# Kernel tuning notes

Hardware: AMD Instinct MI355X
Metric: run time of the kernel (lower is better)

Reference implementation:

```python
import jax, jax.numpy as jnp
import numpy as np

N = 4096
IN_FEATS = 64
HIDDEN = 128
STEPS = 3
SCALE = 3.0
LJ_EPS = 0.1
LJ_SIGMA = 3.5
LJ_MIX = 0.1  # 'auto' branch: pot = exp(-r/scale)*relu(score) + 0.1*lj
LN_EPS = 1e-5


def setup_inputs() -> dict:
    key = jax.random.key(0)
    ks = jax.random.split(key, 12)
    x = jax.random.normal(ks[0], (N, IN_FEATS), dtype=jnp.float32)
    # sparse-ish 0/1 adjacency (float, as multiplied in the torch code)
    adj = (jax.random.uniform(ks[1], (N, N)) < 0.02).astype(jnp.float32)
    # positive pairwise distances in Angstrom-like range
    dist_mat = jax.random.uniform(ks[2], (N, N), dtype=jnp.float32) * 10.0 + 0.5
    s_in = 1.0 / np.sqrt(IN_FEATS)
    s_h = 1.0 / np.sqrt(HIDDEN)
    s_2h = 1.0 / np.sqrt(2 * HIDDEN)
    params = {
        'W_in': jax.random.uniform(ks[3], (IN_FEATS, HIDDEN), minval=-s_in, maxval=s_in),
        'b_in': jnp.zeros((HIDDEN,), jnp.float32),
        'W_msg': jax.random.uniform(ks[4], (HIDDEN, HIDDEN), minval=-s_h, maxval=s_h),
        'b_msg': jnp.zeros((HIDDEN,), jnp.float32),
        'W_u1': jax.random.uniform(ks[5], (2 * HIDDEN, HIDDEN), minval=-s_2h, maxval=s_2h),
        'b_u1': jnp.zeros((HIDDEN,), jnp.float32),
        'W_u2': jax.random.uniform(ks[6], (HIDDEN, HIDDEN), minval=-s_h, maxval=s_h),
        'b_u2': jnp.zeros((HIDDEN,), jnp.float32),
        'gamma': jnp.ones((HIDDEN,), jnp.float32),
        'beta': jnp.zeros((HIDDEN,), jnp.float32),
    }
    return {'x': x, 'adj': adj, 'dist_mat': dist_mat, **params}


def _layernorm(x, gamma, beta):
    mu = jnp.mean(x, axis=-1, keepdims=True)
    var = jnp.mean(jnp.square(x - mu), axis=-1, keepdims=True)
    return (x - mu) * jax.lax.rsqrt(var + LN_EPS) * gamma + beta


def reference(x, adj, dist_mat, W_in, b_in, W_msg, b_msg, W_u1, b_u1, W_u2, b_u2, gamma, beta):
    h = x @ W_in + b_in  # (n, hidden)
    # distance-only terms are loop-invariant
    r_safe = jnp.clip(dist_mat, 1e-6, None)
    sr6 = (LJ_SIGMA / r_safe) ** 6
    lj = 4.0 * LJ_EPS * (sr6 * sr6 - sr6)          # (n, n)
    decay = jnp.exp(-dist_mat / SCALE)             # (n, n)
    pot_const = LJ_MIX * lj                        # 'auto' branch constant part
    for _ in range(STEPS):
        # torch code computes msg_lin(h) but never uses it (dead code) -> skipped
        # pot_scalar[i,j] = <h_i, h_j>, computed without (n,n,d) materialization
        pot_scalar = h @ h.T                       # (n, n)
        pot = decay * jax.nn.relu(pot_scalar) + pot_const
        # m_i = sum_j pot[i,j]*adj[i,j]*h_j == masked-weighted matmul
        m = (pot * adj) @ h                        # (n, hidden)
        concat = jnp.concatenate([h, m], axis=-1)  # (n, 2*hidden)
        delta = jax.nn.relu(concat @ W_u1 + b_u1) @ W_u2 + b_u2
        h = _layernorm(h + delta, gamma, beta)
    return h
```

## Files before the change

### kernel.cpp

```cpp
#include <hip/hip_runtime.h>
#include <hip/hip_bf16.h>

#define NN   4096
#define HID  128
#define INFE 64
#define KE   160
#define KMAX 192
#define CH   64
#define RPB  4

typedef unsigned short u16;
typedef unsigned int   u32;

__device__ __forceinline__ float bfu(u16 u) { return __uint_as_float(((u32)u) << 16); }
__device__ __forceinline__ float bflo(u32 w){ return __uint_as_float(w << 16); }
__device__ __forceinline__ float bfhi(u32 w){ return __uint_as_float(w & 0xffff0000u); }
__device__ __forceinline__ u16 f2b(float f) { __hip_bfloat16 h = __float2bfloat16(f); return *(u16*)&h; }

__global__ __launch_bounds__(128) void k_h0(
    const float* __restrict__ x, const float* __restrict__ Win, const float* __restrict__ bin,
    float* __restrict__ hdst, u16* __restrict__ bdst)
{
    __shared__ float xl[INFE];
    const int r = blockIdx.x;
    const int d = threadIdx.x;
    if (d < INFE) xl[d] = x[(size_t)r*INFE + d];
    __syncthreads();
    float acc = bin[d];
    #pragma unroll 8
    for (int k = 0; k < INFE; ++k)
        acc = fmaf(xl[k], Win[k*HID + d], acc);
    hdst[(size_t)r*HID + d] = acc;
    bdst[(size_t)r*HID + d] = f2b(acc);
}

__global__ __launch_bounds__(256) void k_build(
    const float* __restrict__ adj, const float* __restrict__ dist,
    float4* __restrict__ edges, int* __restrict__ nnzp)
{
    __shared__ int cnt[2];
    __shared__ int   cl[2][KE];
    __shared__ float ca[2][KE];
    const int r0 = blockIdx.x * 2;
    const int t  = threadIdx.x;
    if (t < 2) cnt[t] = 0;
    __syncthreads();
    float4 av[2][4];
    #pragma unroll
    for (int rr = 0; rr < 2; ++rr) {
        const float4* arow = (const float4*)(adj + (size_t)(r0+rr)*NN);
        #pragma unroll
        for (int q = 0; q < 4; ++q) av[rr][q] = arow[t + 256*q];
    }
    #pragma unroll
    for (int rr = 0; rr < 2; ++rr) {
        #pragma unroll
        for (int q = 0; q < 4; ++q) {
            float a4[4] = {av[rr][q].x, av[rr][q].y, av[rr][q].z, av[rr][q].w};
            if (a4[0] != 0.f || a4[1] != 0.f || a4[2] != 0.f || a4[3] != 0.f) {
                #pragma unroll
                for (int u = 0; u < 4; ++u) {
                    if (a4[u] != 0.f) {
                        int pos = atomicAdd(&cnt[rr], 1);
                        if (pos < KE) { cl[rr][pos] = 4*(t + 256*q) + u; ca[rr][pos] = a4[u]; }
                    }
                }
            }
        }
    }
    __syncthreads();
    #pragma unroll
    for (int rr = 0; rr < 2; ++rr) {
        const int n  = cnt[rr] < KE ? cnt[rr] : KE;
        const int np = (n + 15) / 16 * 16;
        float4* erow = edges + (size_t)(r0+rr)*KE;
        for (int i = n + t; i < np; i += 256)
            erow[i] = make_float4(__int_as_float(0), 0.f, 0.f, 0.f);
        const float* drow = dist + (size_t)(r0+rr)*NN;
        for (int i = t; i < n; i += 256) {
            int   c = cl[rr][i];
            float a = ca[rr][i];
            float d  = fmaxf(drow[c], 1e-6f);
            float dw1 = a * __expf(-d * (1.0f/3.0f));
            float tt = 3.5f / d, t2 = tt*tt, t6 = t2*t2*t2;
            float dw2 = a * 0.04f * (t6*t6 - t6);
            erow[i] = make_float4(__int_as_float(c), dw1, dw2, 0.f);
        }
        if (t == 0) nnzp[r0+rr] = np;
    }
}

__global__ __launch_bounds__(256) void k_fstep(
    const float4* __restrict__ edges, const int* __restrict__ nnzp,
    const float* __restrict__ h, const u16* __restrict__ hb,
    const float* __restrict__ Wu1, const float* __restrict__ bu1,
    const float* __restrict__ Wu2, const float* __restrict__ bu2,
    const float* __restrict__ gam, const float* __restrict__ bet,
    float* __restrict__ hout, u16* __restrict__ bout)
{
    __shared__ __align__(16) float4 eds[RPB][KE];
    __shared__ int npl[RPB];
    __shared__ __align__(16) float hs[RPB][HID];
    __shared__ __align__(16) float ms[RPB][HID];
    __shared__ __align__(16) float h1s[RPB][HID];
    __shared__ float hn[RPB][HID];
    const int t    = threadIdx.x;
    const int w    = t >> 6;
    const int lane = t & 63;
    const int g    = lane >> 5;
    const int j    = lane & 31;
    const int r0   = blockIdx.x * RPB;
    const int r    = r0 + w;

    if (t < RPB) npl[t] = nnzp[r0 + t];
    const float4 hi4 = *(const float4*)(h + (size_t)r*HID + 4*j);
    if (g == 0) *(float4*)&hs[w][4*j] = hi4;
    __syncthreads();
    #pragma unroll
    for (int rr = 0; rr < RPB; ++rr) {
        const float4* er = edges + (size_t)(r0+rr)*KE;
        for (int i = t; i < npl[rr]; i += 256) eds[rr][i] = er[i];
    }
    __syncthreads();

    const int np = npl[w];
    float4 macc = make_float4(0.f, 0.f, 0.f, 0.f);
    for (int e0 = 0; e0 < np; e0 += 16) {
        float4 ed[8]; uint2 hj16[8]; float p[8];
        #pragma unroll
        for (int q = 0; q < 8; ++q) ed[q] = eds[w][e0 + g + 2*q];
        #pragma unroll
        for (int q = 0; q < 8; ++q) {
            int c = __float_as_int(ed[q].x);
            hj16[q] = *(const uint2*)(hb + (size_t)c*HID + 4*j);
        }
        float4 hjf[8];
        #pragma unroll
        for (int q = 0; q < 8; ++q) {
            hjf[q].x = bflo(hj16[q].x); hjf[q].y = bfhi(hj16[q].x);
            hjf[q].z = bflo(hj16[q].y); hjf[q].w = bfhi(hj16[q].y);
            p[q] = hi4.x*hjf[q].x;
            p[q] = fmaf(hi4.y, hjf[q].y, p[q]);
            p[q] = fmaf(hi4.z, hjf[q].z, p[q]);
            p[q] = fmaf(hi4.w, hjf[q].w, p[q]);
        }
        #pragma unroll
        for (int mask = 1; mask <= 16; mask <<= 1) {
            #pragma unroll
            for (int q = 0; q < 8; ++q) p[q] += __shfl_xor(p[q], mask);
        }
        #pragma unroll
        for (int q = 0; q < 8; ++q) {
            float wq = fmaf(ed[q].y, fmaxf(p[q], 0.f), ed[q].z);
            macc.x = fmaf(wq, hjf[q].x, macc.x);
            macc.y = fmaf(wq, hjf[q].y, macc.y);
            macc.z = fmaf(wq, hjf[q].z, macc.z);
            macc.w = fmaf(wq, hjf[q].w, macc.w);
        }
    }
    macc.x += __shfl_xor(macc.x, 32);
    macc.y += __shfl_xor(macc.y, 32);
    macc.z += __shfl_xor(macc.z, 32);
    macc.w += __shfl_xor(macc.w, 32);
    if (g == 0) *(float4*)&ms[w][4*j] = macc;
    __syncthreads();

    {
        const int half = t >> 7;
        const int d    = t & 127;
        const int ra = 2*half, rb = ra + 1;
        float bb = bu1[d];
        float a0 = bb, a1 = bb;
        for (int k = 0; k < HID; k += 4) {
            float w0 = Wu1[(k+0)*HID + d], w1 = Wu1[(k+1)*HID + d];
            float w2 = Wu1[(k+2)*HID + d], w3 = Wu1[(k+3)*HID + d];
            float4 caa = *(const float4*)&hs[ra][k];
            float4 cbb = *(const float4*)&hs[rb][k];
            a0 = fmaf(caa.x,w0,a0); a0 = fmaf(caa.y,w1,a0); a0 = fmaf(caa.z,w2,a0); a0 = fmaf(caa.w,w3,a0);
            a1 = fmaf(cbb.x,w0,a1); a1 = fmaf(cbb.y,w1,a1); a1 = fmaf(cbb.z,w2,a1); a1 = fmaf(cbb.w,w3,a1);
        }
        for (int k = 0; k < HID; k += 4) {
            float w0 = Wu1[(HID+k+0)*HID + d], w1 = Wu1[(HID+k+1)*HID + d];
            float w2 = Wu1[(HID+k+2)*HID + d], w3 = Wu1[(HID+k+3)*HID + d];
            float4 caa = *(const float4*)&ms[ra][k];
            float4 cbb = *(const float4*)&ms[rb][k];
            a0 = fmaf(caa.x,w0,a0); a0 = fmaf(caa.y,w1,a0); a0 = fmaf(caa.z,w2,a0); a0 = fmaf(caa.w,w3,a0);
            a1 = fmaf(cbb.x,w0,a1); a1 = fmaf(cbb.y,w1,a1); a1 = fmaf(cbb.z,w2,a1); a1 = fmaf(cbb.w,w3,a1);
        }
        h1s[ra][d] = fmaxf(a0, 0.f);
        h1s[rb][d] = fmaxf(a1, 0.f);
    }
    __syncthreads();
    {
        const int half = t >> 7;
        const int d    = t & 127;
        const int ra = 2*half, rb = ra + 1;
        float bb = bu2[d];
        float b0 = bb, b1 = bb;
        for (int k = 0; k < HID; k += 4) {
            float w0 = Wu2[(k+0)*HID + d], w1 = Wu2[(k+1)*HID + d];
            float w2 = Wu2[(k+2)*HID + d], w3 = Wu2[(k+3)*HID + d];
            float4 caa = *(const float4*)&h1s[ra][k];
            float4 cbb = *(const float4*)&h1s[rb][k];
            b0 = fmaf(caa.x,w0,b0); b0 = fmaf(caa.y,w1,b0); b0 = fmaf(caa.z,w2,b0); b0 = fmaf(caa.w,w3,b0);
            b1 = fmaf(cbb.x,w0,b1); b1 = fmaf(cbb.y,w1,b1); b1 = fmaf(cbb.z,w2,b1); b1 = fmaf(cbb.w,w3,b1);
        }
        hn[ra][d] = hs[ra][d] + b0;
        hn[rb][d] = hs[rb][d] + b1;
    }
    __syncthreads();
    {
        float v0 = hn[w][lane], v1 = hn[w][lane + 64];
        float s = v0 + v1;
        #pragma unroll
        for (int mask = 1; mask <= 32; mask <<= 1) s += __shfl_xor(s, mask);
        float mu = s * (1.0f/128.0f);
        float z0 = v0 - mu, z1 = v1 - mu;
        float vv = fmaf(z0, z0, z1*z1);
        #pragma unroll
        for (int mask = 1; mask <= 32; mask <<= 1) vv += __shfl_xor(vv, mask);
        float rstd = rsqrtf(vv * (1.0f/128.0f) + 1e-5f);
        float o0 = fmaf(z0 * rstd, gam[lane],      bet[lane]);
        float o1 = fmaf(z1 * rstd, gam[lane + 64], bet[lane + 64]);
        hout[(size_t)r*HID + lane]      = o0;
        hout[(size_t)r*HID + lane + 64] = o1;
        bout[(size_t)r*HID + lane]      = f2b(o0);
        bout[(size_t)r*HID + lane + 64] = f2b(o1);
    }
}

template<bool SB, bool DB>
__global__ __launch_bounds__(128) void k_step(
    const float* __restrict__ adj, const float* __restrict__ dist,
    const void* hsrc, void* hdst,
    const float* __restrict__ Wu1, const float* __restrict__ bu1,
    const float* __restrict__ Wu2, const float* __restrict__ bu2,
    const float* __restrict__ gam, const float* __restrict__ bet)
{
    __shared__ int   cnt4[RPB];
    __shared__ int   cl[RPB][KMAX];
    __shared__ float w1l[RPB][KMAX], w2l[RPB][KMAX];
    __shared__ __align__(16) float hs4[RPB][HID];
    __shared__ __align__(16) float hj[CH][HID + 1];
    __shared__ float pl[CH];
    __shared__ __align__(16) float ms[RPB][HID];
    __shared__ __align__(16) float h1s[RPB][HID];
    __shared__ float hn[RPB][HID];
    const int r0 = blockIdx.x * RPB;
    const int t  = threadIdx.x;
    const u16*   s16 = (const u16*)hsrc;
    const float* s32 = (const float*)hsrc;
    if (t < RPB) cnt4[t] = 0;
    for (int i = t; i < RPB*HID; i += 128) {
        int rr = i >> 7, d = i & 127;
        hs4[rr][d] = SB ? bfu(s16[(size_t)(r0+rr)*HID + d]) : s32[(size_t)(r0+rr)*HID + d];
    }
    __syncthreads();
    for (int idx = t; idx < RPB*(NN/4); idx += 128) {
        int rr = idx >> 10, c4 = idx & 1023;
        float4 a4 = ((const float4*)(adj + (size_t)(r0+rr)*NN))[c4];
        if (a4.x != 0.f || a4.y != 0.f || a4.z != 0.f || a4.w != 0.f) {
            const float* drow = dist + (size_t)(r0+rr)*NN;
            float av4[4] = {a4.x, a4.y, a4.z, a4.w};
            #pragma unroll
            for (int q = 0; q < 4; ++q) {
                float av = av4[q];
                if (av != 0.f) {
                    int c = 4*c4 + q;
                    float d  = fmaxf(drow[c], 1e-6f);
                    float dw1 = av * __expf(-d * (1.0f/3.0f));
                    float tt = 3.5f / d, t2 = tt*tt, t6 = t2*t2*t2;
                    float dw2 = av * 0.04f * (t6*t6 - t6);
                    int pos = atomicAdd(&cnt4[rr], 1);
                    if (pos < KMAX) { cl[rr][pos] = c; w1l[rr][pos] = dw1; w2l[rr][pos] = dw2; }
                }
            }
        }
    }
    __syncthreads();
    int npv[RPB];
    for (int rr = 0; rr < RPB; ++rr) {
        int n  = cnt4[rr] < KMAX ? cnt4[rr] : KMAX;
        int np = (n + CH - 1) / CH * CH;
        npv[rr] = np;
        for (int i = n + t; i < np; i += 128) { cl[rr][i] = 0; w1l[rr][i] = 0.f; w2l[rr][i] = 0.f; }
    }
    __syncthreads();
    const int e2 = t >> 1, hf = t & 1;
    for (int rr = 0; rr < RPB; ++rr) {
        float acc = 0.f;
        for (int e0 = 0; e0 < npv[rr]; e0 += CH) {
            int c = cl[rr][e0 + e2];
            float* dst = &hj[e2][hf*64];
            if (SB) {
                const uint4* sv = (const uint4*)(s16 + (size_t)c*HID + hf*64);
                #pragma unroll
                for (int i = 0; i < 8; ++i) {
                    uint4 v = sv[i];
                    dst[8*i+0] = __uint_as_float(v.x << 16); dst[8*i+1] = __uint_as_float(v.x & 0xffff0000u);
                    dst[8*i+2] = __uint_as_float(v.y << 16); dst[8*i+3] = __uint_as_float(v.y & 0xffff0000u);
                    dst[8*i+4] = __uint_as_float(v.z << 16); dst[8*i+5] = __uint_as_float(v.z & 0xffff0000u);
                    dst[8*i+6] = __uint_as_float(v.w << 16); dst[8*i+7] = __uint_as_float(v.w & 0xffff0000u);
                }
            } else {
                const float4* sv = (const float4*)(s32 + (size_t)c*HID + hf*64);
                #pragma unroll
                for (int i = 0; i < 16; ++i) {
                    float4 v = sv[i];
                    dst[4*i+0] = v.x; dst[4*i+1] = v.y; dst[4*i+2] = v.z; dst[4*i+3] = v.w;
                }
            }
            __syncthreads();
            {
                const float* ha = &hs4[rr][hf*64];
                const float* hb = &hj[e2][hf*64];
                float p = 0.f;
                #pragma unroll
                for (int i = 0; i < 64; ++i) p = fmaf(ha[i], hb[i], p);
                p += __shfl_xor(p, 1);
                if (hf == 0) pl[e2] = fmaf(w1l[rr][e0+e2], fmaxf(p, 0.f), w2l[rr][e0+e2]);
            }
            __syncthreads();
            #pragma unroll
            for (int i = 0; i < CH; ++i) acc = fmaf(pl[i], hj[i][t], acc);
            __syncthreads();
        }
        ms[rr][t] = acc;
    }
    __syncthreads();
    {
        float bb = bu1[t];
        float a0 = bb, a1 = bb, a2 = bb, a3 = bb;
        for (int k = 0; k < HID; k += 4) {
            float w0 = Wu1[(k+0)*HID + t], w1 = Wu1[(k+1)*HID + t];
            float w2 = Wu1[(k+2)*HID + t], w3 = Wu1[(k+3)*HID + t];
            float4 c0 = *(const float4*)&hs4[0][k];
            float4 c1 = *(const float4*)&hs4[1][k];
            float4 c2 = *(const float4*)&hs4[2][k];
            float4 c3 = *(const float4*)&hs4[3][k];
            a0 = fmaf(c0.x,w0,a0); a0 = fmaf(c0.y,w1,a0); a0 = fmaf(c0.z,w2,a0); a0 = fmaf(c0.w,w3,a0);
            a1 = fmaf(c1.x,w0,a1); a1 = fmaf(c1.y,w1,a1); a1 = fmaf(c1.z,w2,a1); a1 = fmaf(c1.w,w3,a1);
            a2 = fmaf(c2.x,w0,a2); a2 = fmaf(c2.y,w1,a2); a2 = fmaf(c2.z,w2,a2); a2 = fmaf(c2.w,w3,a2);
            a3 = fmaf(c3.x,w0,a3); a3 = fmaf(c3.y,w1,a3); a3 = fmaf(c3.z,w2,a3); a3 = fmaf(c3.w,w3,a3);
        }
        for (int k = 0; k < HID; k += 4) {
            float w0 = Wu1[(HID+k+0)*HID + t], w1 = Wu1[(HID+k+1)*HID + t];
            float w2 = Wu1[(HID+k+2)*HID + t], w3 = Wu1[(HID+k+3)*HID + t];
            float4 c0 = *(const float4*)&ms[0][k];
            float4 c1 = *(const float4*)&ms[1][k];
            float4 c2 = *(const float4*)&ms[2][k];
            float4 c3 = *(const float4*)&ms[3][k];
            a0 = fmaf(c0.x,w0,a0); a0 = fmaf(c0.y,w1,a0); a0 = fmaf(c0.z,w2,a0); a0 = fmaf(c0.w,w3,a0);
            a1 = fmaf(c1.x,w0,a1); a1 = fmaf(c1.y,w1,a1); a1 = fmaf(c1.z,w2,a1); a1 = fmaf(c1.w,w3,a1);
            a2 = fmaf(c2.x,w0,a2); a2 = fmaf(c2.y,w1,a2); a2 = fmaf(c2.z,w2,a2); a2 = fmaf(c2.w,w3,a2);
            a3 = fmaf(c3.x,w0,a3); a3 = fmaf(c3.y,w1,a3); a3 = fmaf(c3.z,w2,a3); a3 = fmaf(c3.w,w3,a3);
        }
        h1s[0][t] = fmaxf(a0,0.f); h1s[1][t] = fmaxf(a1,0.f);
        h1s[2][t] = fmaxf(a2,0.f); h1s[3][t] = fmaxf(a3,0.f);
    }
    __syncthreads();
    {
        float bb = bu2[t];
        float b0 = bb, b1 = bb, b2 = bb, b3 = bb;
        for (int k = 0; k < HID; k += 4) {
            float w0 = Wu2[(k+0)*HID + t], w1 = Wu2[(k+1)*HID + t];
            float w2 = Wu2[(k+2)*HID + t], w3 = Wu2[(k+3)*HID + t];
            float4 c0 = *(const float4*)&h1s[0][k];
            float4 c1 = *(const float4*)&h1s[1][k];
            float4 c2 = *(const float4*)&h1s[2][k];
            float4 c3 = *(const float4*)&h1s[3][k];
            b0 = fmaf(c0.x,w0,b0); b0 = fmaf(c0.y,w1,b0); b0 = fmaf(c0.z,w2,b0); b0 = fmaf(c0.w,w3,b0);
            b1 = fmaf(c1.x,w0,b1); b1 = fmaf(c1.y,w1,b1); b1 = fmaf(c1.z,w2,b1); b1 = fmaf(c1.w,w3,b1);
            b2 = fmaf(c2.x,w0,b2); b2 = fmaf(c2.y,w1,b2); b2 = fmaf(c2.z,w2,b2); b2 = fmaf(c2.w,w3,b2);
            b3 = fmaf(c3.x,w0,b3); b3 = fmaf(c3.y,w1,b3); b3 = fmaf(c3.z,w2,b3); b3 = fmaf(c3.w,w3,b3);
        }
        hn[0][t] = hs4[0][t] + b0; hn[1][t] = hs4[1][t] + b1;
        hn[2][t] = hs4[2][t] + b2; hn[3][t] = hs4[3][t] + b3;
    }
    __syncthreads();
    {
        const int lr = t >> 5, j = t & 31;
        float s = 0.f;
        #pragma unroll
        for (int q = 0; q < 4; ++q) s += hn[lr][j + 32*q];
        #pragma unroll
        for (int k2 = 16; k2 >= 1; k2 >>= 1) s += __shfl_xor(s, k2);
        float mu = s * (1.0f/128.0f);
        float v = 0.f;
        #pragma unroll
        for (int q = 0; q < 4; ++q) { float z = hn[lr][j + 32*q] - mu; v = fmaf(z, z, v); }
        #pragma unroll
        for (int k2 = 16; k2 >= 1; k2 >>= 1) v += __shfl_xor(v, k2);
        float rstd = rsqrtf(v * (1.0f/128.0f) + 1e-5f);
        #pragma unroll
        for (int q = 0; q < 4; ++q) {
            int dd = j + 32*q;
            float val = fmaf((hn[lr][dd] - mu) * rstd, gam[dd], bet[dd]);
            if (DB) ((u16*)hdst)[(size_t)(r0+lr)*HID + dd] = f2b(val);
            else    ((float*)hdst)[(size_t)(r0+lr)*HID + dd] = val;
        }
    }
}

extern "C" void kernel_launch(void* const* d_in, const int* in_sizes, int n_in,
                              void* d_out, int out_size, void* d_ws, size_t ws_size,
                              hipStream_t stream)
{
    const float* x    = (const float*)d_in[0];
    const float* adj  = (const float*)d_in[1];
    const float* dist = (const float*)d_in[2];
    const float* Win  = (const float*)d_in[3];
    const float* bin  = (const float*)d_in[4];
    const float* Wu1  = (const float*)d_in[7];
    const float* bu1  = (const float*)d_in[8];
    const float* Wu2  = (const float*)d_in[9];
    const float* bu2  = (const float*)d_in[10];
    const float* gam  = (const float*)d_in[11];
    const float* bet  = (const float*)d_in[12];

    const size_t ebytes = (size_t)NN * KE * sizeof(float4);
    const size_t cbytes = ((size_t)NN * sizeof(int) + 255) & ~255;
    const size_t hb32   = (size_t)NN * HID * sizeof(float);
    const size_t hb16   = (size_t)NN * HID * sizeof(u16);
    const size_t need   = ebytes + cbytes + hb32 + 2*hb16;

    if (ws_size >= need) {
        char* p = (char*)d_ws;
        float4* edges = (float4*)p;            p += ebytes;
        int*    nnzp  = (int*)p;               p += cbytes;
        float*  hA    = (float*)p;             p += hb32;
        u16*    bA    = (u16*)p;               p += hb16;
        u16*    bB    = (u16*)p;               p += hb16;
        float*  hB    = (float*)d_out;

        k_build<<<NN/2, 256, 0, stream>>>(adj, dist, edges, nnzp);
        k_h0<<<NN, 128, 0, stream>>>(x, Win, bin, hA, bA);
        k_fstep<<<NN/RPB, 256, 0, stream>>>(edges, nnzp, hA, bA, Wu1, bu1, Wu2, bu2, gam, bet, hB, bB);
        k_fstep<<<NN/RPB, 256, 0, stream>>>(edges, nnzp, hB, bB, Wu1, bu1, Wu2, bu2, gam, bet, hA, bA);
        k_fstep<<<NN/RPB, 256, 0, stream>>>(edges, nnzp, hA, bA, Wu1, bu1, Wu2, bu2, gam, bet, hB, bB);
    } else if (ws_size >= hb32) {
        void* A = d_ws; void* B = d_out;
        hipLaunchKernelGGL((k_step<false,false>), dim3(NN/RPB), dim3(128), 0, stream,
                           adj, dist, A, B, Wu1, bu1, Wu2, bu2, gam, bet);
    }
    if (ws_size < need) {
        const size_t hb = hb32;
        if (ws_size >= hb) {
            void* A = d_ws; void* B = d_out;
            k_h0<<<NN, 128, 0, stream>>>(x, Win, bin, (float*)A, (u16*)((char*)A + hb - hb16));
            k_step<false,false><<<NN/RPB, 128, 0, stream>>>(adj, dist, A, B, Wu1, bu1, Wu2, bu2, gam, bet);
            k_step<false,false><<<NN/RPB, 128, 0, stream>>>(adj, dist, B, A, Wu1, bu1, Wu2, bu2, gam, bet);
            k_step<false,false><<<NN/RPB, 128, 0, stream>>>(adj, dist, A, B, Wu1, bu1, Wu2, bu2, gam, bet);
        }
    }
}
```

Baseline: 264.4 us.

## Fuse edge build with input projection; process 8 rows per step block with split-K MLP

Merges the edge-list build and the initial h projection into one launch, removing a kernel launch. The step kernel now handles 8 rows per 512-thread block. Its two dense MLP layers are split along K across four thread groups, each holding 8 row accumulators, and the partial sums are reduced through shared memory. This reuses each weight load across 8 rows instead of 2, cutting global weight traffic. In exchange it uses more shared memory and registers per block, adds extra barriers, and launches half as many blocks.

```diff
diff --git a/kernel.cpp b/kernel.cpp
--- a/kernel.cpp
+++ b/kernel.cpp
@@ -8,6 +8,7 @@
 #define KMAX 192
 #define CH   64
 #define RPB  4
+#define RPB8 8
 
 typedef unsigned short u16;
 typedef unsigned int   u32;
@@ -34,63 +35,80 @@
     bdst[(size_t)r*HID + d] = f2b(acc);
 }
 
-__global__ __launch_bounds__(256) void k_build(
+__global__ __launch_bounds__(256) void k_prep(
     const float* __restrict__ adj, const float* __restrict__ dist,
-    float4* __restrict__ edges, int* __restrict__ nnzp)
+    float4* __restrict__ edges, int* __restrict__ nnzp,
+    const float* __restrict__ x, const float* __restrict__ Win, const float* __restrict__ bin,
+    float* __restrict__ hdst, u16* __restrict__ bdst)
 {
-    __shared__ int cnt[2];
-    __shared__ int   cl[2][KE];
-    __shared__ float ca[2][KE];
-    const int r0 = blockIdx.x * 2;
-    const int t  = threadIdx.x;
-    if (t < 2) cnt[t] = 0;
-    __syncthreads();
-    float4 av[2][4];
-    #pragma unroll
-    for (int rr = 0; rr < 2; ++rr) {
-        const float4* arow = (const float4*)(adj + (size_t)(r0+rr)*NN);
-        #pragma unroll
-        for (int q = 0; q < 4; ++q) av[rr][q] = arow[t + 256*q];
-    }
-    #pragma unroll
-    for (int rr = 0; rr < 2; ++rr) {
-        #pragma unroll
-        for (int q = 0; q < 4; ++q) {
-            float a4[4] = {av[rr][q].x, av[rr][q].y, av[rr][q].z, av[rr][q].w};
-            if (a4[0] != 0.f || a4[1] != 0.f || a4[2] != 0.f || a4[3] != 0.f) {
-                #pragma unroll
-                for (int u = 0; u < 4; ++u) {
-                    if (a4[u] != 0.f) {
-                        int pos = atomicAdd(&cnt[rr], 1);
-                        if (pos < KE) { cl[rr][pos] = 4*(t + 256*q) + u; ca[rr][pos] = a4[u]; }
+    const int t = threadIdx.x;
+    if (blockIdx.x < NN/2) {
+        __shared__ int cnt[2];
+        __shared__ int   cl[2][KE];
+        __shared__ float ca[2][KE];
+        const int r0 = blockIdx.x * 2;
+        if (t < 2) cnt[t] = 0;
+        __syncthreads();
+        float4 av[2][4];
+        #pragma unroll
+        for (int rr = 0; rr < 2; ++rr) {
+            const float4* arow = (const float4*)(adj + (size_t)(r0+rr)*NN);
+            #pragma unroll
+            for (int q = 0; q < 4; ++q) av[rr][q] = arow[t + 256*q];
+        }
+        #pragma unroll
+        for (int rr = 0; rr < 2; ++rr) {
+            #pragma unroll
+            for (int q = 0; q < 4; ++q) {
+                float a4[4] = {av[rr][q].x, av[rr][q].y, av[rr][q].z, av[rr][q].w};
+                if (a4[0] != 0.f || a4[1] != 0.f || a4[2] != 0.f || a4[3] != 0.f) {
+                    #pragma unroll
+                    for (int u = 0; u < 4; ++u) {
+                        if (a4[u] != 0.f) {
+                            int pos = atomicAdd(&cnt[rr], 1);
+                            if (pos < KE) { cl[rr][pos] = 4*(t + 256*q) + u; ca[rr][pos] = a4[u]; }
+                        }
                     }
                 }
             }
         }
-    }
-    __syncthreads();
-    #pragma unroll
-    for (int rr = 0; rr < 2; ++rr) {
-        const int n  = cnt[rr] < KE ? cnt[rr] : KE;
-        const int np = (n + 15) / 16 * 16;
-        float4* erow = edges + (size_t)(r0+rr)*KE;
-        for (int i = n + t; i < np; i += 256)
-            erow[i] = make_float4(__int_as_float(0), 0.f, 0.f, 0.f);
-        const float* drow = dist + (size_t)(r0+rr)*NN;
-        for (int i = t; i < n; i += 256) {
-            int   c = cl[rr][i];
-            float a = ca[rr][i];
-            float d  = fmaxf(drow[c], 1e-6f);
-            float dw1 = a * __expf(-d * (1.0f/3.0f));
-            float tt = 3.5f / d, t2 = tt*tt, t6 = t2*t2*t2;
-            float dw2 = a * 0.04f * (t6*t6 - t6);
-            erow[i] = make_float4(__int_as_float(c), dw1, dw2, 0.f);
-        }
-        if (t == 0) nnzp[r0+rr] = np;
+        __syncthreads();
+        #pragma unroll
+        for (int rr = 0; rr < 2; ++rr) {
+            const int n  = cnt[rr] < KE ? cnt[rr] : KE;
+            const int np = (n + 15) / 16 * 16;
+            float4* erow = edges + (size_t)(r0+rr)*KE;
+            for (int i = n + t; i < np; i += 256)
+                erow[i] = make_float4(__int_as_float(0), 0.f, 0.f, 0.f);
+            const float* drow = dist + (size_t)(r0+rr)*NN;
+            for (int i = t; i < n; i += 256) {
+                int   c = cl[rr][i];
+                float a = ca[rr][i];
+                float d  = fmaxf(drow[c], 1e-6f);
+                float dw1 = a * __expf(-d * (1.0f/3.0f));
+                float tt = 3.5f / d, t2 = tt*tt, t6 = t2*t2*t2;
+                float dw2 = a * 0.04f * (t6*t6 - t6);
+                erow[i] = make_float4(__int_as_float(c), dw1, dw2, 0.f);
+            }
+            if (t == 0) nnzp[r0+rr] = np;
+        }
+    } else {
+        __shared__ float xl[2][INFE];
+        const int grp = t >> 7;
+        const int d   = t & 127;
+        const int r   = (blockIdx.x - NN/2) * 2 + grp;
+        if (d < INFE) xl[grp][d] = x[(size_t)r*INFE + d];
+        __syncthreads();
+        float acc = bin[d];
+        #pragma unroll 8
+        for (int k = 0; k < INFE; ++k)
+            acc = fmaf(xl[grp][k], Win[k*HID + d], acc);
+        hdst[(size_t)r*HID + d] = acc;
+        bdst[(size_t)r*HID + d] = f2b(acc);
     }
 }
 
-__global__ __launch_bounds__(256) void k_fstep(
+__global__ __launch_bounds__(512, 4) void k_fstep8(
     const float4* __restrict__ edges, const int* __restrict__ nnzp,
     const float* __restrict__ h, const u16* __restrict__ hb,
     const float* __restrict__ Wu1, const float* __restrict__ bu1,
@@ -98,28 +116,28 @@
     const float* __restrict__ gam, const float* __restrict__ bet,
     float* __restrict__ hout, u16* __restrict__ bout)
 {
-    __shared__ __align__(16) float4 eds[RPB][KE];
-    __shared__ int npl[RPB];
-    __shared__ __align__(16) float hs[RPB][HID];
-    __shared__ __align__(16) float ms[RPB][HID];
-    __shared__ __align__(16) float h1s[RPB][HID];
-    __shared__ float hn[RPB][HID];
+    __shared__ __align__(16) float4 eds[RPB8][KE];
+    __shared__ int npl[RPB8];
+    __shared__ __align__(16) float hs[RPB8][HID];
+    __shared__ __align__(16) float ms[RPB8][HID];
+    __shared__ __align__(16) float h1s[RPB8][HID];
+    __shared__ float hn[RPB8][HID];
+    __shared__ float ps[4][RPB8][HID];
     const int t    = threadIdx.x;
     const int w    = t >> 6;
     const int lane = t & 63;
     const int g    = lane >> 5;
     const int j    = lane & 31;
-    const int r0   = blockIdx.x * RPB;
+    const int r0   = blockIdx.x * RPB8;
     const int r    = r0 + w;
 
-    if (t < RPB) npl[t] = nnzp[r0 + t];
+    if (t < RPB8) npl[t] = nnzp[r0 + t];
     const float4 hi4 = *(const float4*)(h + (size_t)r*HID + 4*j);
     if (g == 0) *(float4*)&hs[w][4*j] = hi4;
     __syncthreads();
-    #pragma unroll
-    for (int rr = 0; rr < RPB; ++rr) {
-        const float4* er = edges + (size_t)(r0+rr)*KE;
-        for (int i = t; i < npl[rr]; i += 256) eds[rr][i] = er[i];
+    for (int i = t; i < RPB8*KE; i += 512) {
+        int rr = i / KE, c = i - rr*KE;
+        if (c < npl[rr]) eds[rr][c] = edges[(size_t)(r0+rr)*KE + c];
     }
     __syncthreads();
 
@@ -166,47 +184,66 @@
     __syncthreads();
 
     {
-        const int half = t >> 7;
-        const int d    = t & 127;
-        const int ra = 2*half, rb = ra + 1;
-        float bb = bu1[d];
-        float a0 = bb, a1 = bb;
-        for (int k = 0; k < HID; k += 4) {
-            float w0 = Wu1[(k+0)*HID + d], w1 = Wu1[(k+1)*HID + d];
-            float w2 = Wu1[(k+2)*HID + d], w3 = Wu1[(k+3)*HID + d];
-            float4 caa = *(const float4*)&hs[ra][k];
-            float4 cbb = *(const float4*)&hs[rb][k];
-            a0 = fmaf(caa.x,w0,a0); a0 = fmaf(caa.y,w1,a0); a0 = fmaf(caa.z,w2,a0); a0 = fmaf(caa.w,w3,a0);
-            a1 = fmaf(cbb.x,w0,a1); a1 = fmaf(cbb.y,w1,a1); a1 = fmaf(cbb.z,w2,a1); a1 = fmaf(cbb.w,w3,a1);
-        }
-        for (int k = 0; k < HID; k += 4) {
-            float w0 = Wu1[(HID+k+0)*HID + d], w1 = Wu1[(HID+k+1)*HID + d];
-            float w2 = Wu1[(HID+k+2)*HID + d], w3 = Wu1[(HID+k+3)*HID + d];
-            float4 caa = *(const float4*)&ms[ra][k];
-            float4 cbb = *(const float4*)&ms[rb][k];
-            a0 = fmaf(caa.x,w0,a0); a0 = fmaf(caa.y,w1,a0); a0 = fmaf(caa.z,w2,a0); a0 = fmaf(caa.w,w3,a0);
-            a1 = fmaf(cbb.x,w0,a1); a1 = fmaf(cbb.y,w1,a1); a1 = fmaf(cbb.z,w2,a1); a1 = fmaf(cbb.w,w3,a1);
-        }
-        h1s[ra][d] = fmaxf(a0, 0.f);
-        h1s[rb][d] = fmaxf(a1, 0.f);
-    }
-    __syncthreads();
-    {
-        const int half = t >> 7;
-        const int d    = t & 127;
-        const int ra = 2*half, rb = ra + 1;
-        float bb = bu2[d];
-        float b0 = bb, b1 = bb;
-        for (int k = 0; k < HID; k += 4) {
-            float w0 = Wu2[(k+0)*HID + d], w1 = Wu2[(k+1)*HID + d];
-            float w2 = Wu2[(k+2)*HID + d], w3 = Wu2[(k+3)*HID + d];
-            float4 caa = *(const float4*)&h1s[ra][k];
-            float4 cbb = *(const float4*)&h1s[rb][k];
-            b0 = fmaf(caa.x,w0,b0); b0 = fmaf(caa.y,w1,b0); b0 = fmaf(caa.z,w2,b0); b0 = fmaf(caa.w,w3,b0);
-            b1 = fmaf(cbb.x,w0,b1); b1 = fmaf(cbb.y,w1,b1); b1 = fmaf(cbb.z,w2,b1); b1 = fmaf(cbb.w,w3,b1);
-        }
-        hn[ra][d] = hs[ra][d] + b0;
-        hn[rb][d] = hs[rb][d] + b1;
+        const int kq = t >> 7;
+        const int d  = t & 127;
+        const float binit = (kq == 0) ? bu1[d] : 0.f;
+        float acc[RPB8];
+        #pragma unroll
+        for (int rr = 0; rr < RPB8; ++rr) acc[rr] = binit;
+        const float (*src)[HID] = (kq < 2) ? hs : ms;
+        const int kb = (kq & 1) * 64;
+        const float* wp = Wu1 + (size_t)kq * 64 * HID + d;
+        #pragma unroll 2
+        for (int k = 0; k < 64; k += 4) {
+            float w0 = wp[(k+0)*HID], w1 = wp[(k+1)*HID];
+            float w2 = wp[(k+2)*HID], w3 = wp[(k+3)*HID];
+            #pragma unroll
+            for (int rr = 0; rr < RPB8; ++rr) {
+                float4 c4 = *(const float4*)&src[rr][kb + k];
+                acc[rr] = fmaf(c4.x, w0, acc[rr]);
+                acc[rr] = fmaf(c4.y, w1, acc[rr]);
+                acc[rr] = fmaf(c4.z, w2, acc[rr]);
+                acc[rr] = fmaf(c4.w, w3, acc[rr]);
+            }
+        }
+        #pragma unroll
+        for (int rr = 0; rr < RPB8; ++rr) ps[kq][rr][d] = acc[rr];
+    }
+    __syncthreads();
+    for (int pidx = t; pidx < RPB8*HID; pidx += 512) {
+        int rr = pidx >> 7, d = pidx & 127;
+        h1s[rr][d] = fmaxf(ps[0][rr][d] + ps[1][rr][d] + ps[2][rr][d] + ps[3][rr][d], 0.f);
+    }
+    __syncthreads();
+    {
+        const int kq = t >> 7;
+        const int d  = t & 127;
+        const float binit = (kq == 0) ? bu2[d] : 0.f;
+        float acc[RPB8];
+        #pragma unroll
+        for (int rr = 0; rr < RPB8; ++rr) acc[rr] = binit;
+        const int kb = kq * 32;
+        const float* wp = Wu2 + (size_t)kq * 32 * HID + d;
+        #pragma unroll 2
+        for (int k = 0; k < 32; k += 4) {
+            float w0 = wp[(k+0)*HID], w1 = wp[(k+1)*HID];
+            float w2 = wp[(k+2)*HID], w3 = wp[(k+3)*HID];
+            #pragma unroll
+            for (int rr = 0; rr < RPB8; ++rr) {
+                float4 c4 = *(const float4*)&h1s[rr][kb + k];
+                acc[rr] = fmaf(c4.x, w0, acc[rr]);
+                acc[rr] = fmaf(c4.y, w1, acc[rr]);
+                acc[rr] = fmaf(c4.z, w2, acc[rr]);
+                acc[rr] = fmaf(c4.w, w3, acc[rr]);
+            }
+        }
+        #pragma unroll
+        for (int rr = 0; rr < RPB8; ++rr) ps[kq][rr][d] = acc[rr];
+    }
+    __syncthreads();
+    for (int pidx = t; pidx < RPB8*HID; pidx += 512) {
+        int rr = pidx >> 7, d = pidx & 127;
+        hn[rr][d] = hs[rr][d] + ps[0][rr][d] + ps[1][rr][d] + ps[2][rr][d] + ps[3][rr][d];
     }
     __syncthreads();
     {
@@ -433,24 +470,15 @@
         u16*    bB    = (u16*)p;               p += hb16;
         float*  hB    = (float*)d_out;
 
-        k_build<<<NN/2, 256, 0, stream>>>(adj, dist, edges, nnzp);
-        k_h0<<<NN, 128, 0, stream>>>(x, Win, bin, hA, bA);
-        k_fstep<<<NN/RPB, 256, 0, stream>>>(edges, nnzp, hA, bA, Wu1, bu1, Wu2, bu2, gam, bet, hB, bB);
-        k_fstep<<<NN/RPB, 256, 0, stream>>>(edges, nnzp, hB, bB, Wu1, bu1, Wu2, bu2, gam, bet, hA, bA);
-        k_fstep<<<NN/RPB, 256, 0, stream>>>(edges, nnzp, hA, bA, Wu1, bu1, Wu2, bu2, gam, bet, hB, bB);
+        k_prep<<<NN, 256, 0, stream>>>(adj, dist, edges, nnzp, x, Win, bin, hA, bA);
+        k_fstep8<<<NN/RPB8, 512, 0, stream>>>(edges, nnzp, hA, bA, Wu1, bu1, Wu2, bu2, gam, bet, hB, bB);
+        k_fstep8<<<NN/RPB8, 512, 0, stream>>>(edges, nnzp, hB, bB, Wu1, bu1, Wu2, bu2, gam, bet, hA, bA);
+        k_fstep8<<<NN/RPB8, 512, 0, stream>>>(edges, nnzp, hA, bA, Wu1, bu1, Wu2, bu2, gam, bet, hB, bB);
     } else if (ws_size >= hb32) {
         void* A = d_ws; void* B = d_out;
-        hipLaunchKernelGGL((k_step<false,false>), dim3(NN/RPB), dim3(128), 0, stream,
-                           adj, dist, A, B, Wu1, bu1, Wu2, bu2, gam, bet);
-    }
-    if (ws_size < need) {
-        const size_t hb = hb32;
-        if (ws_size >= hb) {
-            void* A = d_ws; void* B = d_out;
-            k_h0<<<NN, 128, 0, stream>>>(x, Win, bin, (float*)A, (u16*)((char*)A + hb - hb16));
-            k_step<false,false><<<NN/RPB, 128, 0, stream>>>(adj, dist, A, B, Wu1, bu1, Wu2, bu2, gam, bet);
-            k_step<false,false><<<NN/RPB, 128, 0, stream>>>(adj, dist, B, A, Wu1, bu1, Wu2, bu2, gam, bet);
-            k_step<false,false><<<NN/RPB, 128, 0, stream>>>(adj, dist, A, B, Wu1, bu1, Wu2, bu2, gam, bet);
-        }
+        k_h0<<<NN, 128, 0, stream>>>(x, Win, bin, (float*)A, (u16*)B);
+        k_step<false,false><<<NN/RPB, 128, 0, stream>>>(adj, dist, A, B, Wu1, bu1, Wu2, bu2, gam, bet);
+        k_step<false,false><<<NN/RPB, 128, 0, stream>>>(adj, dist, B, A, Wu1, bu1, Wu2, bu2, gam, bet);
+        k_step<false,false><<<NN/RPB, 128, 0, stream>>>(adj, dist, A, B, Wu1, bu1, Wu2, bu2, gam, bet);
     }
 }
```

Result: faster. 252.4 us (-4.5%).
